# Kernel optimization log

Measured on AMD Instinct MI355X. Metric: run time of the kernel, lower is better.

Reference implementation:

```python
import jax, jax.numpy as jnp
import numpy as np

N_NODES, N_EDGES, D_IN, N_GRAPHS = 20000, 320000, 256, 32
H1, C1, H2, C2 = 4, 128, 4, 64


def setup_inputs() -> dict:
    key = jax.random.key(0)
    ks = jax.random.split(key, 24)
    g = lambda k, shape, fan: jax.random.normal(k, shape, jnp.float32) * (1.0 / np.sqrt(fan))
    inp = {
        'x': jax.random.normal(ks[0], (N_NODES, D_IN), jnp.float32),
        'edge_index': jax.random.randint(ks[1], (2, N_EDGES), 0, N_NODES, jnp.int32),
        'batch': jnp.sort(jax.random.randint(ks[2], (N_NODES,), 0, N_GRAPHS, jnp.int32)),
        'edge_attr': jax.random.normal(ks[3], (N_EDGES, 1), jnp.float32),
        # GATConv 1: lin [D_IN, H1*C1], att_src/dst/edge [H1,C1], lin_edge [1,H1*C1], bias [H1*C1]
        'W1': g(ks[4], (D_IN, H1 * C1), D_IN),
        'as1': g(ks[5], (H1, C1), C1),
        'ad1': g(ks[6], (H1, C1), C1),
        'We1': g(ks[7], (1, H1 * C1), 1),
        'ae1': g(ks[8], (H1, C1), C1),
        'b1': jnp.zeros((H1 * C1,), jnp.float32),
        'g1': jnp.ones((H1 * C1,), jnp.float32),
        'be1': jnp.zeros((H1 * C1,), jnp.float32),
        # GATConv 2 (concat=False -> out 64)
        'W2': g(ks[9], (H1 * C1, H2 * C2), H1 * C1),
        'as2': g(ks[10], (H2, C2), C2),
        'ad2': g(ks[11], (H2, C2), C2),
        'We2': g(ks[12], (1, H2 * C2), 1),
        'ae2': g(ks[13], (H2, C2), C2),
        'b2': jnp.zeros((C2,), jnp.float32),
        'g2': jnp.ones((C2,), jnp.float32),
        'be2': jnp.zeros((C2,), jnp.float32),
        'fw1': g(ks[14], (C2, 32), C2),
        'fb1': jnp.zeros((32,), jnp.float32),
        'fw2': g(ks[15], (32, 1), 32),
        'fb2': jnp.zeros((1,), jnp.float32),
    }
    return inp


def _gat(x, src, dst, ea, W, a_s, a_d, We, a_e, bias, H, C, concat, n):
    h = (x @ W).reshape(n, H, C)                         # [N,H,C]
    al_s = jnp.einsum('nhc,hc->nh', h, a_s)              # [N,H]
    al_d = jnp.einsum('nhc,hc->nh', h, a_d)
    e = (ea @ We).reshape(-1, H, C)                      # [E',H,C]
    al_e = jnp.einsum('ehc,hc->eh', e, a_e)
    logits = jax.nn.leaky_relu(al_s[src] + al_d[dst] + al_e, 0.2)  # [E',H]
    m = jax.ops.segment_max(logits, dst, num_segments=n)
    m = jnp.where(jnp.isfinite(m), m, 0.0)
    p = jnp.exp(logits - m[dst])
    denom = jax.ops.segment_sum(p, dst, num_segments=n)
    alpha = p / (denom[dst] + 1e-16)                     # segment softmax
    out = jax.ops.segment_sum(h[src] * alpha[:, :, None], dst, num_segments=n)
    out = out.reshape(n, H * C) if concat else out.mean(axis=1)
    return out + bias


def _bn(x, gamma, beta):
    mu = x.mean(axis=0)
    var = x.var(axis=0)
    return gamma * (x - mu) * jax.lax.rsqrt(var + 1e-5) + beta


def reference(x, edge_index, batch, edge_attr, W1, as1, ad1, We1, ae1, b1, g1, be1,
              W2, as2, ad2, We2, ae2, b2, g2, be2, fw1, fb1, fw2, fb2):
    n = x.shape[0]
    loop = jnp.arange(n, dtype=edge_index.dtype)
    src = jnp.concatenate([edge_index[0], loop])
    dst = jnp.concatenate([edge_index[1], loop])
    # self-loop edge_attr filled with mean (PyG fill_value='mean')
    ea = jnp.concatenate([edge_attr, jnp.broadcast_to(edge_attr.mean(axis=0), (n, edge_attr.shape[1]))])

    h = _gat(x, src, dst, ea, W1, as1, ad1, We1, ae1, b1, H1, C1, True, n)
    h = jax.nn.elu(_bn(h, g1, be1))
    h = _gat(h, src, dst, ea, W2, as2, ad2, We2, ae2, b2, H2, C2, False, n)
    h = jax.nn.elu(_bn(h, g2, be2))

    sums = jax.ops.segment_sum(h, batch, num_segments=N_GRAPHS)
    cnt = jax.ops.segment_sum(jnp.ones((n,), h.dtype), batch, num_segments=N_GRAPHS)
    pooled = sums / jnp.maximum(cnt, 1.0)[:, None]       # global_mean_pool
    # dropout is identity in eval mode
    out = jax.nn.elu(pooled @ fw1 + fb1) @ fw2 + fb2
    return out
```

## Files before the change

kernel.cpp:

```cpp
#include <hip/hip_runtime.h>
#include <hip/hip_bf16.h>

#define N_NODES  20000
#define MPAD     20096
#define N_EDGES  320000
#define N_EP     (N_EDGES + N_NODES)
#define D_IN     256
#define N_GRAPHS 32
#define HH1 4
#define CC1 128
#define HH2 4
#define CC2 64

#define R1_OFF     0ull
#define R2_OFF     41156608ull
#define XB_OFF     61734912ull
#define ALPHA_OFF  72024064ull
#define EAF_OFF    77464064ull
#define W1BT_OFF   78744064ull
#define W2BT_OFF   79006208ull
#define CSR_OFF    79268352ull
#define DEG_OFF    81988352ull
#define MUSUM_OFF  82068352ull
#define M2SUM_OFF  82070400ull
#define POOL_OFF   82072448ull
#define FLAGZ_OFF  82080640ull
#define EAACC_OFF  82080768ull
#define ZERO0_START DEG_OFF
#define ZERO0_SIZE  92480ull
#define ROWPTR_OFF 82080832ull
#define ALS_OFF    82160896ull
#define ALD_OFF    82480896ull
#define MU_OFF     82800896ull
#define RSTD_OFF   82802944ull
#define SBUF_OFF   82804992ull
#define SMALL_OFF  82805056ull
#define H1_OFF     R1_OFF
#define OUT1_OFF   R1_OFF
#define H2_OFF     R1_OFF
#define HB2_OFF    (R1_OFF + 20578304ull)
#define HB1_OFF    R2_OFF
#define OUT1B_OFF  R2_OFF
#define OUT2A_OFF  R2_OFF
#define OUT2_OFF   ALPHA_OFF

#define S_AS1 0
#define S_AD1 512
#define S_WE1 1024
#define S_AE1 1536
#define S_G1  2048
#define S_BE1 2560
#define S_AS2 3072
#define S_AD2 3328
#define S_WE2 3584
#define S_AE2 3840
#define S_G2  4096
#define S_BE2 4160
#define S_FW1 4224
#define S_FB1 6272
#define S_FW2 6304
#define S_FB2 6336

typedef __attribute__((ext_vector_type(8))) short bf8_t;
typedef __attribute__((ext_vector_type(4))) float f4_t;

__global__ void detect_dtype(const unsigned short* __restrict__ xr, int* __restrict__ flag) {
    int i = blockIdx.x * blockDim.x + threadIdx.x;
    unsigned short u = xr[i];
    if ((u & 0x7F80) == 0x7F80) atomicOr(flag, 1);
}

__device__ __forceinline__ float loadF(const void* p, int i, int fp32) {
    return fp32 ? ((const float*)p)[i]
                : __bfloat162float(((const __hip_bfloat16*)p)[i]);
}

__global__ void cvt_big(const int* __restrict__ flag, const void* __restrict__ src,
                        float* __restrict__ dst, int n) {
    int fp32 = flag[0];
    for (int i = blockIdx.x * blockDim.x + threadIdx.x; i < n; i += gridDim.x * blockDim.x)
        dst[i] = loadF(src, i, fp32);
}

__global__ void cvt_to_bf16(const int* __restrict__ flag, const void* __restrict__ src,
                            __hip_bfloat16* __restrict__ dst, int n_valid, int n_total) {
    int i = blockIdx.x * blockDim.x + threadIdx.x;
    if (i >= n_total) return;
    float v = (i < n_valid) ? loadF(src, i, flag[0]) : 0.f;
    dst[i] = __float2bfloat16(v);
}

__global__ void cvt_w_t(const int* __restrict__ flag, const void* __restrict__ W,
                        __hip_bfloat16* __restrict__ Wt, int K, int N) {
    int i = blockIdx.x * blockDim.x + threadIdx.x;
    if (i >= K * N) return;
    int k = i / N, n = i % N;
    Wt[(size_t)n * K + k] = __float2bfloat16(loadF(W, i, flag[0]));
}

__global__ void cvt_smalls(const int* __restrict__ flag, float* __restrict__ dst,
                           const void* as1, const void* ad1, const void* We1, const void* ae1,
                           const void* g1, const void* be1, const void* as2, const void* ad2,
                           const void* We2, const void* ae2, const void* g2, const void* be2,
                           const void* fw1, const void* fb1, const void* fw2, const void* fb2) {
    const void* srcs[16] = {as1, ad1, We1, ae1, g1, be1, as2, ad2, We2, ae2, g2, be2, fw1, fb1, fw2, fb2};
    const int cnts[16] = {512, 512, 512, 512, 512, 512, 256, 256, 256, 256, 64, 64, 2048, 32, 32, 1};
    const int offs[16] = {S_AS1, S_AD1, S_WE1, S_AE1, S_G1, S_BE1, S_AS2, S_AD2,
                          S_WE2, S_AE2, S_G2, S_BE2, S_FW1, S_FB1, S_FW2, S_FB2};
    int b = blockIdx.x;
    int fp32 = flag[0];
    for (int i = threadIdx.x; i < cnts[b]; i += blockDim.x)
        dst[offs[b] + i] = loadF(srcs[b], i, fp32);
}

__global__ void ea_reduce(const float* __restrict__ ea, float* __restrict__ acc) {
    __shared__ float sh[256];
    float s = 0.f;
    for (int i = blockIdx.x * blockDim.x + threadIdx.x; i < N_EDGES; i += gridDim.x * blockDim.x)
        s += ea[i];
    sh[threadIdx.x] = s;
    __syncthreads();
    for (int st = 128; st; st >>= 1) {
        if (threadIdx.x < st) sh[threadIdx.x] += sh[threadIdx.x + st];
        __syncthreads();
    }
    if (threadIdx.x == 0) atomicAdd(acc, sh[0]);
}

__global__ void compute_s(const float* __restrict__ smalls, float* __restrict__ sbuf) {
    int t = threadIdx.x;
    if (t < 4) {
        float s = 0.f;
        for (int c = 0; c < CC1; ++c) s += smalls[S_WE1 + t * CC1 + c] * smalls[S_AE1 + t * CC1 + c];
        sbuf[t] = s;
    } else if (t < 8) {
        int h = t - 4;
        float s = 0.f;
        for (int c = 0; c < CC2; ++c) s += smalls[S_WE2 + h * CC2 + c] * smalls[S_AE2 + h * CC2 + c];
        sbuf[t] = s;
    }
}

__global__ void edge_hist(const int* __restrict__ ei, int* __restrict__ deg) {
    int e = blockIdx.x * blockDim.x + threadIdx.x;
    if (e >= N_EP) return;
    int d = (e < N_EDGES) ? ei[N_EDGES + e] : e - N_EDGES;
    atomicAdd(&deg[d], 1);
}

__global__ void deg_scan(const int* __restrict__ deg, int* __restrict__ rowptr) {
    __shared__ int part[256];
    int t = threadIdx.x;
    int lo = t * 79;
    int hi = lo + 79; if (hi > N_NODES) hi = N_NODES; if (lo > N_NODES) lo = N_NODES;
    int s = 0;
    for (int i = lo; i < hi; ++i) s += deg[i];
    part[t] = s;
    __syncthreads();
    for (int off = 1; off < 256; off <<= 1) {
        int u = (t >= off) ? part[t - off] : 0;
        __syncthreads();
        if (t >= off) part[t] += u;
        __syncthreads();
    }
    int run = part[t] - s;
    for (int i = lo; i < hi; ++i) { rowptr[i] = run; run += deg[i]; }
    if (hi == N_NODES && lo < N_NODES) rowptr[N_NODES] = run;
}

__global__ void edge_scatter(const int* __restrict__ ei, const int* __restrict__ rowptr,
                             int* __restrict__ cursor, int2* __restrict__ csr_se) {
    int e = blockIdx.x * blockDim.x + threadIdx.x;
    if (e >= N_EP) return;
    int s, d;
    if (e < N_EDGES) { s = ei[e]; d = ei[N_EDGES + e]; }
    else { s = d = e - N_EDGES; }
    int pos = rowptr[d] + atomicAdd(&cursor[d], 1);
    csr_se[pos] = make_int2(s, e);
}

__global__ void graph_bounds(const int* __restrict__ batch, int* __restrict__ gstart) {
    int i = blockIdx.x * blockDim.x + threadIdx.x;
    if (i >= N_NODES) return;
    int b = batch[i];
    if (i == 0) {
        for (int g = 0; g <= b; ++g) gstart[g] = 0;
    } else {
        int pb = batch[i - 1];
        for (int g = pb + 1; g <= b; ++g) gstart[g] = i;
    }
    if (i == N_NODES - 1) {
        for (int g = b + 1; g <= N_GRAPHS; ++g) gstart[g] = N_NODES;
    }
}

__global__ __launch_bounds__(256) void gemm_mfma(
        const short* __restrict__ A, const short* __restrict__ Bt,
        float* __restrict__ C, __hip_bfloat16* __restrict__ Cb, int N, int K) {
    __shared__ short As[128 * 40];
    __shared__ short Bs[64 * 40];
    int t = threadIdx.x;
    int wv = t >> 6, lane = t & 63, quad = lane >> 4, lr = lane & 15;
    int m0 = blockIdx.y * 128, n0 = blockIdx.x * 64;
    f4_t acc[2][4] = {};
    int ra0 = t >> 2, sa0 = t & 3;
    int ra1 = (t + 256) >> 2, sa1 = t & 3;
    for (int k0 = 0; k0 < K; k0 += 32) {
        *(uint4*)&As[ra0 * 40 + sa0 * 8] = *(const uint4*)&A[(size_t)(m0 + ra0) * K + k0 + sa0 * 8];
        *(uint4*)&As[ra1 * 40 + sa1 * 8] = *(const uint4*)&A[(size_t)(m0 + ra1) * K + k0 + sa1 * 8];
        *(uint4*)&Bs[ra0 * 40 + sa0 * 8] = *(const uint4*)&Bt[(size_t)(n0 + ra0) * K + k0 + sa0 * 8];
        __syncthreads();
        bf8_t a0 = *(const bf8_t*)&As[(wv * 16 + lr) * 40 + quad * 8];
        bf8_t a1 = *(const bf8_t*)&As[((wv + 4) * 16 + lr) * 40 + quad * 8];
#pragma unroll
        for (int nt = 0; nt < 4; ++nt) {
            bf8_t b = *(const bf8_t*)&Bs[(nt * 16 + lr) * 40 + quad * 8];
            acc[0][nt] = __builtin_amdgcn_mfma_f32_16x16x32_bf16(a0, b, acc[0][nt], 0, 0, 0);
            acc[1][nt] = __builtin_amdgcn_mfma_f32_16x16x32_bf16(a1, b, acc[1][nt], 0, 0, 0);
        }
        __syncthreads();
    }
#pragma unroll
    for (int si = 0; si < 2; ++si) {
        int mrow = m0 + (wv + si * 4) * 16 + quad * 4;
#pragma unroll
        for (int nt = 0; nt < 4; ++nt) {
            int col = n0 + nt * 16 + lr;
#pragma unroll
            for (int r = 0; r < 4; ++r) {
                float v = acc[si][nt][r];
                C[(size_t)(mrow + r) * N + col] = v;
                Cb[(size_t)(mrow + r) * N + col] = __float2bfloat16(v);
            }
        }
    }
}

__global__ void al_kernel(const float* __restrict__ hbuf, const float* __restrict__ smalls,
                          int s_as, int s_ad,
                          float* __restrict__ als, float* __restrict__ ald, int H, int C) {
    int n = blockIdx.x;
    int lane = threadIdx.x;
    int HC = H * C;
    for (int h = 0; h < H; ++h) {
        float ss = 0.f, sd = 0.f;
        for (int c = lane; c < C; c += 64) {
            float v = hbuf[(size_t)n * HC + h * C + c];
            ss += v * smalls[s_as + h * C + c];
            sd += v * smalls[s_ad + h * C + c];
        }
        for (int off = 32; off; off >>= 1) {
            ss += __shfl_down(ss, off);
            sd += __shfl_down(sd, off);
        }
        if (lane == 0) { als[n * H + h] = ss; ald[n * H + h] = sd; }
    }
}

__global__ __launch_bounds__(64) void edge_softmax_csr(
        const int* __restrict__ rowptr, const int2* __restrict__ csr_se,
        const float* __restrict__ als, const float* __restrict__ ald,
        const float* __restrict__ eaf, const float* __restrict__ ea_acc,
        const float* __restrict__ sbuf, float* __restrict__ alpha) {
    int d = blockIdx.x;
    int lane = threadIdx.x;
    int beg = rowptr[d], end = rowptr[d + 1];
    float ea_mean = ea_acc[0] * (1.0f / N_EDGES);
    float4 ad = *(const float4*)&ald[d * 4];
    float s0 = sbuf[0], s1 = sbuf[1], s2 = sbuf[2], s3 = sbuf[3];
    float m0 = -INFINITY, m1 = -INFINITY, m2 = -INFINITY, m3 = -INFINITY;
    for (int p = beg + lane; p < end; p += 64) {
        int2 se = csr_se[p];
        float eav = (se.y < N_EDGES) ? eaf[se.y] : ea_mean;
        float4 as = *(const float4*)&als[se.x * 4];
        float l0 = as.x + ad.x + eav * s0; l0 = l0 > 0.f ? l0 : 0.2f * l0;
        float l1 = as.y + ad.y + eav * s1; l1 = l1 > 0.f ? l1 : 0.2f * l1;
        float l2 = as.z + ad.z + eav * s2; l2 = l2 > 0.f ? l2 : 0.2f * l2;
        float l3 = as.w + ad.w + eav * s3; l3 = l3 > 0.f ? l3 : 0.2f * l3;
        float4 lv = {l0, l1, l2, l3};
        *(float4*)&alpha[(size_t)p * 4] = lv;
        m0 = fmaxf(m0, l0); m1 = fmaxf(m1, l1); m2 = fmaxf(m2, l2); m3 = fmaxf(m3, l3);
    }
#pragma unroll
    for (int off = 1; off < 64; off <<= 1) {
        m0 = fmaxf(m0, __shfl_xor(m0, off));
        m1 = fmaxf(m1, __shfl_xor(m1, off));
        m2 = fmaxf(m2, __shfl_xor(m2, off));
        m3 = fmaxf(m3, __shfl_xor(m3, off));
    }
    float t0 = 0.f, t1 = 0.f, t2 = 0.f, t3 = 0.f;
    for (int p = beg + lane; p < end; p += 64) {
        float4 lv = *(const float4*)&alpha[(size_t)p * 4];
        lv.x = __expf(lv.x - m0); lv.y = __expf(lv.y - m1);
        lv.z = __expf(lv.z - m2); lv.w = __expf(lv.w - m3);
        *(float4*)&alpha[(size_t)p * 4] = lv;
        t0 += lv.x; t1 += lv.y; t2 += lv.z; t3 += lv.w;
    }
#pragma unroll
    for (int off = 1; off < 64; off <<= 1) {
        t0 += __shfl_xor(t0, off);
        t1 += __shfl_xor(t1, off);
        t2 += __shfl_xor(t2, off);
        t3 += __shfl_xor(t3, off);
    }
    float r0 = 1.0f / (t0 + 1e-16f), r1 = 1.0f / (t1 + 1e-16f);
    float r2 = 1.0f / (t2 + 1e-16f), r3 = 1.0f / (t3 + 1e-16f);
    for (int p = beg + lane; p < end; p += 64) {
        float4 lv = *(const float4*)&alpha[(size_t)p * 4];
        lv.x *= r0; lv.y *= r1; lv.z *= r2; lv.w *= r3;
        *(float4*)&alpha[(size_t)p * 4] = lv;
    }
}

template <int HC, int C>
__global__ __launch_bounds__(HC / 4) void agg_csr_bf(
        const int* __restrict__ rowptr, const int2* __restrict__ csr_se,
        const float* __restrict__ alpha, const __hip_bfloat16* __restrict__ hb,
        float* __restrict__ outb) {
    int d = blockIdx.x;
    int t = threadIdx.x;
    int h = (4 * t) / C;
    float a0 = 0.f, a1 = 0.f, a2 = 0.f, a3 = 0.f;
    int beg = rowptr[d], end = rowptr[d + 1];
    for (int p = beg; p < end; ++p) {
        int2 se = csr_se[p];
        float w = alpha[(size_t)p * 4 + h];
        uint2 raw = *(const uint2*)&hb[(size_t)se.x * HC + 4 * t];
        a0 += w * __uint_as_float(raw.x << 16);
        a1 += w * __uint_as_float(raw.x & 0xFFFF0000u);
        a2 += w * __uint_as_float(raw.y << 16);
        a3 += w * __uint_as_float(raw.y & 0xFFFF0000u);
    }
    float4 v = {a0, a1, a2, a3};
    *(float4*)&outb[(size_t)d * HC + 4 * t] = v;
}

__global__ void bn_part(const float* __restrict__ x, float* __restrict__ musum, float* __restrict__ m2sum, int Cc) {
    int c = threadIdx.x;
    float s = 0.f, s2 = 0.f;
    for (int i = blockIdx.x; i < N_NODES; i += gridDim.x) {
        float v = x[(size_t)i * Cc + c];
        s += v; s2 += v * v;
    }
    atomicAdd(&musum[c], s);
    atomicAdd(&m2sum[c], s2);
}

__global__ void bn_fin(float* __restrict__ musum, float* __restrict__ m2sum,
                       float* __restrict__ mu, float* __restrict__ rstd, int Cc) {
    int c = threadIdx.x;
    if (c >= Cc) return;
    float m = musum[c] / N_NODES;
    float var = m2sum[c] / N_NODES - m * m;
    mu[c] = m;
    rstd[c] = rsqrtf(var + 1e-5f);
    musum[c] = 0.f;
    m2sum[c] = 0.f;
}

__global__ void bn_apply_elu_b(const float* __restrict__ x, const float* __restrict__ mu,
                               const float* __restrict__ rstd, const float* __restrict__ smalls,
                               int s_g, int s_be, __hip_bfloat16* __restrict__ out,
                               int total, int Cc) {
    int i = blockIdx.x * blockDim.x + threadIdx.x;
    if (i >= total) return;
    int j = i % Cc;
    float y = smalls[s_g + j] * (x[i] - mu[j]) * rstd[j] + smalls[s_be + j];
    y = y > 0.f ? y : expm1f(y);
    out[i] = __float2bfloat16(y);
}

__global__ void bn_apply_elu(float* __restrict__ x, const float* __restrict__ mu, const float* __restrict__ rstd,
                             const float* __restrict__ smalls, int s_g, int s_be,
                             int total, int Cc) {
    int i = blockIdx.x * blockDim.x + threadIdx.x;
    if (i >= total) return;
    int j = i % Cc;
    float y = smalls[s_g + j] * (x[i] - mu[j]) * rstd[j] + smalls[s_be + j];
    x[i] = y > 0.f ? y : expm1f(y);
}

__global__ void head_mean(const float* __restrict__ ina, float* __restrict__ outb) {
    int i = blockIdx.x * blockDim.x + threadIdx.x;
    if (i >= N_NODES * CC2) return;
    int nd = i / CC2, c = i % CC2;
    float s = 0.f;
#pragma unroll
    for (int h = 0; h < HH2; ++h) s += ina[(size_t)nd * (HH2 * CC2) + h * CC2 + c];
    outb[i] = s * (1.0f / HH2);
}

__global__ __launch_bounds__(256) void pool_seg(const float* __restrict__ x, const int* __restrict__ gstart,
                                                float* __restrict__ pooled) {
    int g = blockIdx.x;
    int c = threadIdx.x & 63;
    int j = threadIdx.x >> 6;
    int beg = gstart[g], end = gstart[g + 1];
    float s = 0.f;
    for (int i = beg + j; i < end; i += 4)
        s += x[(size_t)i * CC2 + c];
    __shared__ float sh[4][64];
    sh[j][c] = s;
    __syncthreads();
    if (j == 0) {
        float tot = sh[0][c] + sh[1][c] + sh[2][c] + sh[3][c];
        float n = (float)(end - beg);
        pooled[g * CC2 + c] = tot / fmaxf(n, 1.0f);
    }
}

__global__ void mlp_kernel(const float* __restrict__ pooled,
                           const float* __restrict__ smalls, const int* __restrict__ flag,
                           void* __restrict__ outp) {
    int g = blockIdx.x;
    int k = threadIdx.x;
    __shared__ float hsh[32];
    float acc = smalls[S_FB1 + k];
    for (int c = 0; c < CC2; ++c)
        acc += pooled[g * CC2 + c] * smalls[S_FW1 + c * 32 + k];
    acc = acc > 0.f ? acc : expm1f(acc);
    hsh[k] = acc;
    __syncthreads();
    if (k == 0) {
        float o = smalls[S_FB2];
        for (int t = 0; t < 32; ++t) o += hsh[t] * smalls[S_FW2 + t];
        if (flag[0]) ((float*)outp)[g] = o;
        else ((__hip_bfloat16*)outp)[g] = __float2bfloat16(o);
    }
}

extern "C" void kernel_launch(void* const* d_in, const int* in_sizes, int n_in,
                              void* d_out, int out_size, void* d_ws, size_t ws_size,
                              hipStream_t stream) {
    const void* x    = d_in[0];
    const int* ei    = (const int*)d_in[1];
    const int* batch = (const int*)d_in[2];
    const void* ea   = d_in[3];
    const void* W1   = d_in[4];
    const void* as1  = d_in[5];
    const void* ad1  = d_in[6];
    const void* We1  = d_in[7];
    const void* ae1  = d_in[8];
    const void* g1   = d_in[10];
    const void* be1  = d_in[11];
    const void* W2   = d_in[12];
    const void* as2  = d_in[13];
    const void* ad2  = d_in[14];
    const void* We2  = d_in[15];
    const void* ae2  = d_in[16];
    const void* g2   = d_in[18];
    const void* be2  = d_in[19];
    const void* fw1  = d_in[20];
    const void* fb1  = d_in[21];
    const void* fw2  = d_in[22];
    const void* fb2  = d_in[23];

    char* ws = (char*)d_ws;
    float* h1      = (float*)(ws + H1_OFF);
    float* out1    = (float*)(ws + OUT1_OFF);
    float* h2      = (float*)(ws + H2_OFF);
    __hip_bfloat16* hb1   = (__hip_bfloat16*)(ws + HB1_OFF);
    __hip_bfloat16* hb2   = (__hip_bfloat16*)(ws + HB2_OFF);
    __hip_bfloat16* out1b = (__hip_bfloat16*)(ws + OUT1B_OFF);
    __hip_bfloat16* xb    = (__hip_bfloat16*)(ws + XB_OFF);
    __hip_bfloat16* W1bt  = (__hip_bfloat16*)(ws + W1BT_OFF);
    __hip_bfloat16* W2bt  = (__hip_bfloat16*)(ws + W2BT_OFF);
    float* out2a   = (float*)(ws + OUT2A_OFF);
    float* out2    = (float*)(ws + OUT2_OFF);
    float* alpha   = (float*)(ws + ALPHA_OFF);
    float* eaf     = (float*)(ws + EAF_OFF);
    int2*  csr_se  = (int2*)(ws + CSR_OFF);
    int*   deg     = (int*)(ws + DEG_OFF);
    float* musum   = (float*)(ws + MUSUM_OFF);
    float* m2sum   = (float*)(ws + M2SUM_OFF);
    float* pooled  = (float*)(ws + POOL_OFF);
    int*   flag    = (int*)(ws + FLAGZ_OFF);
    float* ea_acc  = (float*)(ws + EAACC_OFF);
    int*   rowptr  = (int*)(ws + ROWPTR_OFF);
    float* als     = (float*)(ws + ALS_OFF);
    float* ald     = (float*)(ws + ALD_OFF);
    float* mu      = (float*)(ws + MU_OFF);
    float* rstd    = (float*)(ws + RSTD_OFF);
    float* sbuf    = (float*)(ws + SBUF_OFF);
    float* smalls  = (float*)(ws + SMALL_OFF);
    int*   gstart  = (int*)(ws + DEG_OFF);

    hipMemsetAsync(ws + ZERO0_START, 0, ZERO0_SIZE, stream);

    detect_dtype<<<256, 256, 0, stream>>>((const unsigned short*)x, flag);
    cvt_to_bf16<<<(MPAD * D_IN + 255) / 256, 256, 0, stream>>>(flag, x, xb, N_NODES * D_IN, MPAD * D_IN);
    cvt_big<<<1250, 256, 0, stream>>>(flag, ea, eaf, N_EDGES);
    cvt_w_t<<<512, 256, 0, stream>>>(flag, W1, W1bt, D_IN, HH1 * CC1);
    cvt_w_t<<<512, 256, 0, stream>>>(flag, W2, W2bt, HH1 * CC1, HH2 * CC2);
    cvt_smalls<<<16, 256, 0, stream>>>(flag, smalls, as1, ad1, We1, ae1, g1, be1,
                                       as2, ad2, We2, ae2, g2, be2, fw1, fb1, fw2, fb2);

    ea_reduce<<<256, 256, 0, stream>>>(eaf, ea_acc);
    compute_s<<<1, 64, 0, stream>>>(smalls, sbuf);

    int eb = (N_EP + 255) / 256;
    edge_hist<<<eb, 256, 0, stream>>>(ei, deg);
    deg_scan<<<1, 256, 0, stream>>>(deg, rowptr);
    hipMemsetAsync(ws + DEG_OFF, 0, 80000, stream);
    edge_scatter<<<eb, 256, 0, stream>>>(ei, rowptr, deg, csr_se);
    graph_bounds<<<(N_NODES + 255) / 256, 256, 0, stream>>>(batch, gstart);

    gemm_mfma<<<dim3(512 / 64, MPAD / 128), 256, 0, stream>>>(
        (const short*)xb, (const short*)W1bt, h1, hb1, 512, 256);
    al_kernel<<<N_NODES, 64, 0, stream>>>(h1, smalls, S_AS1, S_AD1, als, ald, HH1, CC1);
    edge_softmax_csr<<<N_NODES, 64, 0, stream>>>(rowptr, csr_se, als, ald, eaf, ea_acc, sbuf, alpha);
    agg_csr_bf<512, 128><<<N_NODES, 128, 0, stream>>>(rowptr, csr_se, alpha, hb1, out1);

    bn_part<<<256, 512, 0, stream>>>(out1, musum, m2sum, 512);
    bn_fin<<<1, 512, 0, stream>>>(musum, m2sum, mu, rstd, 512);
    bn_apply_elu_b<<<(N_NODES * 512 + 255) / 256, 256, 0, stream>>>(
        out1, mu, rstd, smalls, S_G1, S_BE1, out1b, N_NODES * 512, 512);

    gemm_mfma<<<dim3(256 / 64, MPAD / 128), 256, 0, stream>>>(
        (const short*)out1b, (const short*)W2bt, h2, hb2, 256, 512);
    al_kernel<<<N_NODES, 64, 0, stream>>>(h2, smalls, S_AS2, S_AD2, als, ald, HH2, CC2);
    edge_softmax_csr<<<N_NODES, 64, 0, stream>>>(rowptr, csr_se, als, ald, eaf, ea_acc, sbuf + 4, alpha);
    agg_csr_bf<256, 64><<<N_NODES, 64, 0, stream>>>(rowptr, csr_se, alpha, hb2, out2a);

    head_mean<<<(N_NODES * CC2 + 255) / 256, 256, 0, stream>>>(out2a, out2);
    bn_part<<<256, 64, 0, stream>>>(out2, musum, m2sum, 64);
    bn_fin<<<1, 64, 0, stream>>>(musum, m2sum, mu, rstd, 64);
    bn_apply_elu<<<(N_NODES * 64 + 255) / 256, 256, 0, stream>>>(out2, mu, rstd, smalls, S_G2, S_BE2, N_NODES * 64, 64);

    pool_seg<<<N_GRAPHS, 256, 0, stream>>>(out2, gstart, pooled);
    mlp_kernel<<<N_GRAPHS, 32, 0, stream>>>(pooled, smalls, flag, d_out);
}
```

Before: 516.1 us.

## Fuse prep, attention-logit, normalization and pooling kernels; drop fp32 intermediates

Merges the many conversion kernels into one prep launch, folds the attention-logit dot products into the GEMM epilogue through atomics, and moves softmax normalization into the aggregation step, which removes the alpha rewrite pass. Layer-1 aggregation and batchnorm now run on bf16 buffers instead of fp32. The BN finalize step is folded into apply, and pooling is fused with the MLP. The aim is fewer launches and less memory traffic, at the cost of atomic contention in the GEMM epilogue and reduced precision in the intermediates.

```diff
diff --git a/kernel.cpp b/kernel.cpp
--- a/kernel.cpp
+++ b/kernel.cpp
@@ -12,37 +12,36 @@
 #define HH2 4
 #define CC2 64
 
-#define R1_OFF     0ull
-#define R2_OFF     41156608ull
-#define XB_OFF     61734912ull
-#define ALPHA_OFF  72024064ull
-#define EAF_OFF    77464064ull
-#define W1BT_OFF   78744064ull
-#define W2BT_OFF   79006208ull
-#define CSR_OFF    79268352ull
-#define DEG_OFF    81988352ull
-#define MUSUM_OFF  82068352ull
-#define M2SUM_OFF  82070400ull
-#define POOL_OFF   82072448ull
-#define FLAGZ_OFF  82080640ull
-#define EAACC_OFF  82080768ull
+#define XB_OFF      0ull
+#define HB1_OFF     10289152ull
+#define AGG1_OFF    30867456ull
+#define HB2_OFF     51445760ull
+#define OUT2A_OFF   61734912ull
+#define OUT2_OFF    82214912ull
+#define ALPHA_OFF   87334912ull
+#define DENOM_OFF   92774912ull
+#define EAF_OFF     93094912ull
+#define W1BT_OFF    94374912ull
+#define W2BT_OFF    94637056ull
+#define CSR_OFF     94899200ull
+#define ROWPTR_OFF  97619200ull
+#define GSTART_OFF  97699264ull
+#define SMALL_OFF   97699520ull
+#define SBUF_OFF    97725120ull
+#define DEG_OFF     97725184ull
+#define CURS_OFF    97805184ull
+#define ALS1_OFF    97885184ull
+#define ALD1_OFF    98206720ull
+#define ALS2_OFF    98528256ull
+#define ALD2_OFF    98849792ull
+#define MUSUM1_OFF  99171328ull
+#define M2SUM1_OFF  99173376ull
+#define MUSUM2_OFF  99175424ull
+#define M2SUM2_OFF  99175936ull
+#define FLAGZ_OFF   99176448ull
+#define EAACC_OFF   99176576ull
 #define ZERO0_START DEG_OFF
-#define ZERO0_SIZE  92480ull
-#define ROWPTR_OFF 82080832ull
-#define ALS_OFF    82160896ull
-#define ALD_OFF    82480896ull
-#define MU_OFF     82800896ull
-#define RSTD_OFF   82802944ull
-#define SBUF_OFF   82804992ull
-#define SMALL_OFF  82805056ull
-#define H1_OFF     R1_OFF
-#define OUT1_OFF   R1_OFF
-#define H2_OFF     R1_OFF
-#define HB2_OFF    (R1_OFF + 20578304ull)
-#define HB1_OFF    R2_OFF
-#define OUT1B_OFF  R2_OFF
-#define OUT2A_OFF  R2_OFF
-#define OUT2_OFF   ALPHA_OFF
+#define ZERO0_SIZE  1451456ull
 
 #define S_AS1 0
 #define S_AD1 512
@@ -75,89 +74,125 @@
                 : __bfloat162float(((const __hip_bfloat16*)p)[i]);
 }
 
-__global__ void cvt_big(const int* __restrict__ flag, const void* __restrict__ src,
-                        float* __restrict__ dst, int n) {
+#define PB_XB  5024
+#define PB_EAF 313
+#define PB_W   512
+#define PB_SM  16
+#define PREP_BLOCKS (PB_XB + PB_EAF + 2 * PB_W + PB_SM + 1)
+__global__ __launch_bounds__(256) void prep(
+        const int* __restrict__ flag,
+        const void* x, const void* ea, const void* W1, const void* W2,
+        const void* as1, const void* ad1, const void* We1, const void* ae1,
+        const void* g1, const void* be1, const void* as2, const void* ad2,
+        const void* We2, const void* ae2, const void* g2, const void* be2,
+        const void* fw1, const void* fb1, const void* fw2, const void* fb2,
+        __hip_bfloat16* __restrict__ xb, float* __restrict__ eaf, float* __restrict__ ea_acc,
+        __hip_bfloat16* __restrict__ W1bt, __hip_bfloat16* __restrict__ W2bt,
+        float* __restrict__ smalls, float* __restrict__ sbuf) {
+    __shared__ float sh[256];
+    int b = blockIdx.x, t = threadIdx.x;
     int fp32 = flag[0];
-    for (int i = blockIdx.x * blockDim.x + threadIdx.x; i < n; i += gridDim.x * blockDim.x)
-        dst[i] = loadF(src, i, fp32);
-}
-
-__global__ void cvt_to_bf16(const int* __restrict__ flag, const void* __restrict__ src,
-                            __hip_bfloat16* __restrict__ dst, int n_valid, int n_total) {
-    int i = blockIdx.x * blockDim.x + threadIdx.x;
-    if (i >= n_total) return;
-    float v = (i < n_valid) ? loadF(src, i, flag[0]) : 0.f;
-    dst[i] = __float2bfloat16(v);
-}
-
-__global__ void cvt_w_t(const int* __restrict__ flag, const void* __restrict__ W,
-                        __hip_bfloat16* __restrict__ Wt, int K, int N) {
-    int i = blockIdx.x * blockDim.x + threadIdx.x;
-    if (i >= K * N) return;
-    int k = i / N, n = i % N;
-    Wt[(size_t)n * K + k] = __float2bfloat16(loadF(W, i, flag[0]));
-}
-
-__global__ void cvt_smalls(const int* __restrict__ flag, float* __restrict__ dst,
-                           const void* as1, const void* ad1, const void* We1, const void* ae1,
-                           const void* g1, const void* be1, const void* as2, const void* ad2,
-                           const void* We2, const void* ae2, const void* g2, const void* be2,
-                           const void* fw1, const void* fb1, const void* fw2, const void* fb2) {
-    const void* srcs[16] = {as1, ad1, We1, ae1, g1, be1, as2, ad2, We2, ae2, g2, be2, fw1, fb1, fw2, fb2};
-    const int cnts[16] = {512, 512, 512, 512, 512, 512, 256, 256, 256, 256, 64, 64, 2048, 32, 32, 1};
-    const int offs[16] = {S_AS1, S_AD1, S_WE1, S_AE1, S_G1, S_BE1, S_AS2, S_AD2,
-                          S_WE2, S_AE2, S_G2, S_BE2, S_FW1, S_FB1, S_FW2, S_FB2};
-    int b = blockIdx.x;
-    int fp32 = flag[0];
-    for (int i = threadIdx.x; i < cnts[b]; i += blockDim.x)
-        dst[offs[b] + i] = loadF(srcs[b], i, fp32);
-}
-
-__global__ void ea_reduce(const float* __restrict__ ea, float* __restrict__ acc) {
-    __shared__ float sh[256];
-    float s = 0.f;
-    for (int i = blockIdx.x * blockDim.x + threadIdx.x; i < N_EDGES; i += gridDim.x * blockDim.x)
-        s += ea[i];
-    sh[threadIdx.x] = s;
-    __syncthreads();
-    for (int st = 128; st; st >>= 1) {
-        if (threadIdx.x < st) sh[threadIdx.x] += sh[threadIdx.x + st];
+    if (b < PB_XB) {
+        int base = (b * 256 + t) * 4;
+        __hip_bfloat16 tmp[4];
+#pragma unroll
+        for (int j = 0; j < 4; ++j) {
+            int i = base + j;
+            float v = (i < N_NODES * D_IN) ? loadF(x, i, fp32) : 0.f;
+            tmp[j] = __float2bfloat16(v);
+        }
+        *(uint2*)&xb[base] = *(uint2*)tmp;
+        return;
+    }
+    b -= PB_XB;
+    if (b < PB_EAF) {
+        int base = (b * 256 + t) * 4;
+        float s = 0.f;
+#pragma unroll
+        for (int j = 0; j < 4; ++j) {
+            int i = base + j;
+            if (i < N_EDGES) { float v = loadF(ea, i, fp32); eaf[i] = v; s += v; }
+        }
+        sh[t] = s;
         __syncthreads();
-    }
-    if (threadIdx.x == 0) atomicAdd(acc, sh[0]);
-}
-
-__global__ void compute_s(const float* __restrict__ smalls, float* __restrict__ sbuf) {
-    int t = threadIdx.x;
+        for (int st = 128; st; st >>= 1) {
+            if (t < st) sh[t] += sh[t + st];
+            __syncthreads();
+        }
+        if (t == 0) atomicAdd(ea_acc, sh[0]);
+        return;
+    }
+    b -= PB_EAF;
+    if (b < PB_W) {
+        int i = b * 256 + t;
+        int k = i >> 9, n = i & 511;
+        W1bt[(size_t)n * 256 + k] = __float2bfloat16(loadF(W1, i, fp32));
+        return;
+    }
+    b -= PB_W;
+    if (b < PB_W) {
+        int i = b * 256 + t;
+        int k = i >> 8, n = i & 255;
+        W2bt[(size_t)n * 512 + k] = __float2bfloat16(loadF(W2, i, fp32));
+        return;
+    }
+    b -= PB_W;
+    if (b < PB_SM) {
+        const void* srcs[16] = {as1, ad1, We1, ae1, g1, be1, as2, ad2, We2, ae2, g2, be2, fw1, fb1, fw2, fb2};
+        const int cnts[16] = {512, 512, 512, 512, 512, 512, 256, 256, 256, 256, 64, 64, 2048, 32, 32, 1};
+        const int offs[16] = {S_AS1, S_AD1, S_WE1, S_AE1, S_G1, S_BE1, S_AS2, S_AD2,
+                              S_WE2, S_AE2, S_G2, S_BE2, S_FW1, S_FB1, S_FW2, S_FB2};
+        for (int i = t; i < cnts[b]; i += 256)
+            smalls[offs[b] + i] = loadF(srcs[b], i, fp32);
+        return;
+    }
     if (t < 4) {
         float s = 0.f;
-        for (int c = 0; c < CC1; ++c) s += smalls[S_WE1 + t * CC1 + c] * smalls[S_AE1 + t * CC1 + c];
+        for (int c = 0; c < CC1; ++c) s += loadF(We1, t * CC1 + c, fp32) * loadF(ae1, t * CC1 + c, fp32);
         sbuf[t] = s;
     } else if (t < 8) {
         int h = t - 4;
         float s = 0.f;
-        for (int c = 0; c < CC2; ++c) s += smalls[S_WE2 + h * CC2 + c] * smalls[S_AE2 + h * CC2 + c];
-        sbuf[t] = s;
-    }
-}
-
-__global__ void edge_hist(const int* __restrict__ ei, int* __restrict__ deg) {
-    int e = blockIdx.x * blockDim.x + threadIdx.x;
-    if (e >= N_EP) return;
-    int d = (e < N_EDGES) ? ei[N_EDGES + e] : e - N_EDGES;
-    atomicAdd(&deg[d], 1);
-}
-
-__global__ void deg_scan(const int* __restrict__ deg, int* __restrict__ rowptr) {
-    __shared__ int part[256];
+        for (int c = 0; c < CC2; ++c) s += loadF(We2, h * CC2 + c, fp32) * loadF(ae2, h * CC2 + c, fp32);
+        sbuf[4 + h] = s;
+    }
+}
+
+#define HIST_BLOCKS 1329
+__global__ void hist_bounds(const int* __restrict__ ei, int* __restrict__ deg,
+                            const int* __restrict__ batch, int* __restrict__ gstart) {
+    int b = blockIdx.x, t = threadIdx.x;
+    if (b < HIST_BLOCKS) {
+        int e = b * 256 + t;
+        if (e >= N_EP) return;
+        int d = (e < N_EDGES) ? ei[N_EDGES + e] : e - N_EDGES;
+        atomicAdd(&deg[d], 1);
+        return;
+    }
+    int i = (b - HIST_BLOCKS) * 256 + t;
+    if (i >= N_NODES) return;
+    int bb = batch[i];
+    if (i == 0) {
+        for (int g = 0; g <= bb; ++g) gstart[g] = 0;
+    } else {
+        int pb = batch[i - 1];
+        for (int g = pb + 1; g <= bb; ++g) gstart[g] = i;
+    }
+    if (i == N_NODES - 1) {
+        for (int g = bb + 1; g <= N_GRAPHS; ++g) gstart[g] = N_NODES;
+    }
+}
+
+__global__ __launch_bounds__(1024) void deg_scan(const int* __restrict__ deg, int* __restrict__ rowptr) {
+    __shared__ int part[1024];
     int t = threadIdx.x;
-    int lo = t * 79;
-    int hi = lo + 79; if (hi > N_NODES) hi = N_NODES; if (lo > N_NODES) lo = N_NODES;
+    int lo = t * 20;
+    int hi = lo + 20; if (hi > N_NODES) hi = N_NODES; if (lo > N_NODES) lo = N_NODES;
     int s = 0;
     for (int i = lo; i < hi; ++i) s += deg[i];
     part[t] = s;
     __syncthreads();
-    for (int off = 1; off < 256; off <<= 1) {
+    for (int off = 1; off < 1024; off <<= 1) {
         int u = (t >= off) ? part[t - off] : 0;
         __syncthreads();
         if (t >= off) part[t] += u;
@@ -179,24 +214,11 @@
     csr_se[pos] = make_int2(s, e);
 }
 
-__global__ void graph_bounds(const int* __restrict__ batch, int* __restrict__ gstart) {
-    int i = blockIdx.x * blockDim.x + threadIdx.x;
-    if (i >= N_NODES) return;
-    int b = batch[i];
-    if (i == 0) {
-        for (int g = 0; g <= b; ++g) gstart[g] = 0;
-    } else {
-        int pb = batch[i - 1];
-        for (int g = pb + 1; g <= b; ++g) gstart[g] = i;
-    }
-    if (i == N_NODES - 1) {
-        for (int g = b + 1; g <= N_GRAPHS; ++g) gstart[g] = N_NODES;
-    }
-}
-
-__global__ __launch_bounds__(256) void gemm_mfma(
+__global__ __launch_bounds__(256) void gemm_mfma_al(
         const short* __restrict__ A, const short* __restrict__ Bt,
-        float* __restrict__ C, __hip_bfloat16* __restrict__ Cb, int N, int K) {
+        __hip_bfloat16* __restrict__ Cb, int N, int K,
+        float* __restrict__ als, float* __restrict__ ald,
+        const float* __restrict__ asv, const float* __restrict__ adv, int cshift) {
     __shared__ short As[128 * 40];
     __shared__ short Bs[64 * 40];
     int t = threadIdx.x;
@@ -204,10 +226,10 @@
     int m0 = blockIdx.y * 128, n0 = blockIdx.x * 64;
     f4_t acc[2][4] = {};
     int ra0 = t >> 2, sa0 = t & 3;
-    int ra1 = (t + 256) >> 2, sa1 = t & 3;
+    int ra1 = (t + 256) >> 2;
     for (int k0 = 0; k0 < K; k0 += 32) {
         *(uint4*)&As[ra0 * 40 + sa0 * 8] = *(const uint4*)&A[(size_t)(m0 + ra0) * K + k0 + sa0 * 8];
-        *(uint4*)&As[ra1 * 40 + sa1 * 8] = *(const uint4*)&A[(size_t)(m0 + ra1) * K + k0 + sa1 * 8];
+        *(uint4*)&As[ra1 * 40 + sa0 * 8] = *(const uint4*)&A[(size_t)(m0 + ra1) * K + k0 + sa0 * 8];
         *(uint4*)&Bs[ra0 * 40 + sa0 * 8] = *(const uint4*)&Bt[(size_t)(n0 + ra0) * K + k0 + sa0 * 8];
         __syncthreads();
         bf8_t a0 = *(const bf8_t*)&As[(wv * 16 + lr) * 40 + quad * 8];
@@ -227,33 +249,38 @@
         for (int nt = 0; nt < 4; ++nt) {
             int col = n0 + nt * 16 + lr;
 #pragma unroll
-            for (int r = 0; r < 4; ++r) {
-                float v = acc[si][nt][r];
-                C[(size_t)(mrow + r) * N + col] = v;
-                Cb[(size_t)(mrow + r) * N + col] = __float2bfloat16(v);
+            for (int r = 0; r < 4; ++r)
+                Cb[(size_t)(mrow + r) * N + col] = __float2bfloat16(acc[si][nt][r]);
+        }
+    }
+    float asv4[4], adv4[4];
+#pragma unroll
+    for (int nt = 0; nt < 4; ++nt) {
+        asv4[nt] = asv[n0 + nt * 16 + lr];
+        adv4[nt] = adv[n0 + nt * 16 + lr];
+    }
+    int hsel = n0 >> cshift;
+#pragma unroll
+    for (int si = 0; si < 2; ++si) {
+#pragma unroll
+        for (int r = 0; r < 4; ++r) {
+            float ps = 0.f, pd = 0.f;
+#pragma unroll
+            for (int nt = 0; nt < 4; ++nt) {
+                ps += acc[si][nt][r] * asv4[nt];
+                pd += acc[si][nt][r] * adv4[nt];
+            }
+#pragma unroll
+            for (int m = 1; m < 16; m <<= 1) {
+                ps += __shfl_xor(ps, m);
+                pd += __shfl_xor(pd, m);
+            }
+            if (lr == 0) {
+                int row = m0 + (wv + si * 4) * 16 + quad * 4 + r;
+                atomicAdd(&als[row * 4 + hsel], ps);
+                atomicAdd(&ald[row * 4 + hsel], pd);
             }
         }
-    }
-}
-
-__global__ void al_kernel(const float* __restrict__ hbuf, const float* __restrict__ smalls,
-                          int s_as, int s_ad,
-                          float* __restrict__ als, float* __restrict__ ald, int H, int C) {
-    int n = blockIdx.x;
-    int lane = threadIdx.x;
-    int HC = H * C;
-    for (int h = 0; h < H; ++h) {
-        float ss = 0.f, sd = 0.f;
-        for (int c = lane; c < C; c += 64) {
-            float v = hbuf[(size_t)n * HC + h * C + c];
-            ss += v * smalls[s_as + h * C + c];
-            sd += v * smalls[s_ad + h * C + c];
-        }
-        for (int off = 32; off; off >>= 1) {
-            ss += __shfl_down(ss, off);
-            sd += __shfl_down(sd, off);
-        }
-        if (lane == 0) { als[n * H + h] = ss; ald[n * H + h] = sd; }
     }
 }
 
@@ -261,7 +288,7 @@
         const int* __restrict__ rowptr, const int2* __restrict__ csr_se,
         const float* __restrict__ als, const float* __restrict__ ald,
         const float* __restrict__ eaf, const float* __restrict__ ea_acc,
-        const float* __restrict__ sbuf, float* __restrict__ alpha) {
+        const float* __restrict__ sbuf, float* __restrict__ alpha, float* __restrict__ denom) {
     int d = blockIdx.x;
     int lane = threadIdx.x;
     int beg = rowptr[d], end = rowptr[d + 1];
@@ -303,23 +330,21 @@
         t2 += __shfl_xor(t2, off);
         t3 += __shfl_xor(t3, off);
     }
-    float r0 = 1.0f / (t0 + 1e-16f), r1 = 1.0f / (t1 + 1e-16f);
-    float r2 = 1.0f / (t2 + 1e-16f), r3 = 1.0f / (t3 + 1e-16f);
-    for (int p = beg + lane; p < end; p += 64) {
-        float4 lv = *(const float4*)&alpha[(size_t)p * 4];
-        lv.x *= r0; lv.y *= r1; lv.z *= r2; lv.w *= r3;
-        *(float4*)&alpha[(size_t)p * 4] = lv;
-    }
-}
-
-template <int HC, int C>
+    if (lane == 0) {
+        float4 dn = {t0, t1, t2, t3};
+        *(float4*)&denom[d * 4] = dn;
+    }
+}
+
+template <int HC, int C, bool B16OUT>
 __global__ __launch_bounds__(HC / 4) void agg_csr_bf(
         const int* __restrict__ rowptr, const int2* __restrict__ csr_se,
-        const float* __restrict__ alpha, const __hip_bfloat16* __restrict__ hb,
-        float* __restrict__ outb) {
+        const float* __restrict__ alpha, const float* __restrict__ denom,
+        const __hip_bfloat16* __restrict__ hb, void* __restrict__ outb) {
     int d = blockIdx.x;
     int t = threadIdx.x;
     int h = (4 * t) / C;
+    float rdn = 1.0f / (denom[d * (HC / C) + h] + 1e-16f);
     float a0 = 0.f, a1 = 0.f, a2 = 0.f, a3 = 0.f;
     int beg = rowptr[d], end = rowptr[d + 1];
     for (int p = beg; p < end; ++p) {
@@ -331,99 +356,118 @@
         a2 += w * __uint_as_float(raw.y << 16);
         a3 += w * __uint_as_float(raw.y & 0xFFFF0000u);
     }
-    float4 v = {a0, a1, a2, a3};
-    *(float4*)&outb[(size_t)d * HC + 4 * t] = v;
-}
-
-__global__ void bn_part(const float* __restrict__ x, float* __restrict__ musum, float* __restrict__ m2sum, int Cc) {
-    int c = threadIdx.x;
-    float s = 0.f, s2 = 0.f;
+    a0 *= rdn; a1 *= rdn; a2 *= rdn; a3 *= rdn;
+    if (B16OUT) {
+        __hip_bfloat16 tmp[4] = {__float2bfloat16(a0), __float2bfloat16(a1),
+                                 __float2bfloat16(a2), __float2bfloat16(a3)};
+        *(uint2*)&((__hip_bfloat16*)outb)[(size_t)d * HC + 4 * t] = *(uint2*)tmp;
+    } else {
+        float4 v = {a0, a1, a2, a3};
+        *(float4*)&((float*)outb)[(size_t)d * HC + 4 * t] = v;
+    }
+}
+
+__global__ __launch_bounds__(256) void bn_part_b(const __hip_bfloat16* __restrict__ x,
+                                                 float* __restrict__ musum, float* __restrict__ m2sum) {
+    int t = threadIdx.x;
+    float s0 = 0.f, s20 = 0.f, s1 = 0.f, s21 = 0.f;
     for (int i = blockIdx.x; i < N_NODES; i += gridDim.x) {
-        float v = x[(size_t)i * Cc + c];
-        s += v; s2 += v * v;
-    }
-    atomicAdd(&musum[c], s);
-    atomicAdd(&m2sum[c], s2);
-}
-
-__global__ void bn_fin(float* __restrict__ musum, float* __restrict__ m2sum,
-                       float* __restrict__ mu, float* __restrict__ rstd, int Cc) {
-    int c = threadIdx.x;
-    if (c >= Cc) return;
-    float m = musum[c] / N_NODES;
-    float var = m2sum[c] / N_NODES - m * m;
-    mu[c] = m;
-    rstd[c] = rsqrtf(var + 1e-5f);
-    musum[c] = 0.f;
-    m2sum[c] = 0.f;
-}
-
-__global__ void bn_apply_elu_b(const float* __restrict__ x, const float* __restrict__ mu,
-                               const float* __restrict__ rstd, const float* __restrict__ smalls,
-                               int s_g, int s_be, __hip_bfloat16* __restrict__ out,
-                               int total, int Cc) {
+        unsigned u = *(const unsigned*)&x[(size_t)i * 512 + 2 * t];
+        float v0 = __uint_as_float(u << 16);
+        float v1 = __uint_as_float(u & 0xFFFF0000u);
+        s0 += v0; s20 += v0 * v0; s1 += v1; s21 += v1 * v1;
+    }
+    atomicAdd(&musum[2 * t], s0);
+    atomicAdd(&m2sum[2 * t], s20);
+    atomicAdd(&musum[2 * t + 1], s1);
+    atomicAdd(&m2sum[2 * t + 1], s21);
+}
+
+__global__ __launch_bounds__(256) void bn_apply_elu_b16(__hip_bfloat16* __restrict__ x,
+                                                        const float* __restrict__ musum,
+                                                        const float* __restrict__ m2sum,
+                                                        const float* __restrict__ smalls) {
+    int q = blockIdx.x * blockDim.x + threadIdx.x;
+    if (q >= N_NODES * 512 / 4) return;
+    int base = q * 4;
+    int j = base & 511;
+    uint2 raw = *(uint2*)&x[base];
+    float v[4] = {__uint_as_float(raw.x << 16), __uint_as_float(raw.x & 0xFFFF0000u),
+                  __uint_as_float(raw.y << 16), __uint_as_float(raw.y & 0xFFFF0000u)};
+    __hip_bfloat16 tmp[4];
+#pragma unroll
+    for (int k = 0; k < 4; ++k) {
+        int jj = j + k;
+        float m = musum[jj] * (1.0f / N_NODES);
+        float var = m2sum[jj] * (1.0f / N_NODES) - m * m;
+        float y = smalls[S_G1 + jj] * (v[k] - m) * rsqrtf(var + 1e-5f) + smalls[S_BE1 + jj];
+        y = y > 0.f ? y : expm1f(y);
+        tmp[k] = __float2bfloat16(y);
+    }
+    *(uint2*)&x[base] = *(uint2*)tmp;
+}
+
+__global__ __launch_bounds__(256) void head_mean_stats(const float* __restrict__ ina, float* __restrict__ outb,
+                                                       float* __restrict__ musum, float* __restrict__ m2sum) {
+    int t = threadIdx.x;
+    int c = t & 63, j = t >> 6;
+    float ls = 0.f, ls2 = 0.f;
+    for (int nd = blockIdx.x * 4 + j; nd < N_NODES; nd += gridDim.x * 4) {
+        size_t base = (size_t)nd * 256 + c;
+        float s = (ina[base] + ina[base + 64] + ina[base + 128] + ina[base + 192]) * 0.25f;
+        outb[(size_t)nd * 64 + c] = s;
+        ls += s; ls2 += s * s;
+    }
+    __shared__ float shs[4][64], sh2[4][64];
+    shs[j][c] = ls; sh2[j][c] = ls2;
+    __syncthreads();
+    if (j == 0) {
+        atomicAdd(&musum[c], shs[0][c] + shs[1][c] + shs[2][c] + shs[3][c]);
+        atomicAdd(&m2sum[c], sh2[0][c] + sh2[1][c] + sh2[2][c] + sh2[3][c]);
+    }
+}
+
+__global__ void bn_apply_elu_f32(float* __restrict__ x, const float* __restrict__ musum,
+                                 const float* __restrict__ m2sum, const float* __restrict__ smalls) {
     int i = blockIdx.x * blockDim.x + threadIdx.x;
-    if (i >= total) return;
-    int j = i % Cc;
-    float y = smalls[s_g + j] * (x[i] - mu[j]) * rstd[j] + smalls[s_be + j];
-    y = y > 0.f ? y : expm1f(y);
-    out[i] = __float2bfloat16(y);
-}
-
-__global__ void bn_apply_elu(float* __restrict__ x, const float* __restrict__ mu, const float* __restrict__ rstd,
-                             const float* __restrict__ smalls, int s_g, int s_be,
-                             int total, int Cc) {
-    int i = blockIdx.x * blockDim.x + threadIdx.x;
-    if (i >= total) return;
-    int j = i % Cc;
-    float y = smalls[s_g + j] * (x[i] - mu[j]) * rstd[j] + smalls[s_be + j];
+    if (i >= N_NODES * 64) return;
+    int j = i & 63;
+    float m = musum[j] * (1.0f / N_NODES);
+    float var = m2sum[j] * (1.0f / N_NODES) - m * m;
+    float y = smalls[S_G2 + j] * (x[i] - m) * rsqrtf(var + 1e-5f) + smalls[S_BE2 + j];
     x[i] = y > 0.f ? y : expm1f(y);
 }
 
-__global__ void head_mean(const float* __restrict__ ina, float* __restrict__ outb) {
-    int i = blockIdx.x * blockDim.x + threadIdx.x;
-    if (i >= N_NODES * CC2) return;
-    int nd = i / CC2, c = i % CC2;
-    float s = 0.f;
-#pragma unroll
-    for (int h = 0; h < HH2; ++h) s += ina[(size_t)nd * (HH2 * CC2) + h * CC2 + c];
-    outb[i] = s * (1.0f / HH2);
-}
-
-__global__ __launch_bounds__(256) void pool_seg(const float* __restrict__ x, const int* __restrict__ gstart,
-                                                float* __restrict__ pooled) {
+__global__ __launch_bounds__(256) void pool_mlp(const float* __restrict__ x, const int* __restrict__ gstart,
+                                                const float* __restrict__ smalls, const int* __restrict__ flag,
+                                                void* __restrict__ outp) {
     int g = blockIdx.x;
-    int c = threadIdx.x & 63;
-    int j = threadIdx.x >> 6;
+    int t = threadIdx.x;
+    int c = t & 63, j = t >> 6;
     int beg = gstart[g], end = gstart[g + 1];
     float s = 0.f;
     for (int i = beg + j; i < end; i += 4)
-        s += x[(size_t)i * CC2 + c];
+        s += x[(size_t)i * 64 + c];
     __shared__ float sh[4][64];
+    __shared__ float pooled[64];
+    __shared__ float hsh[32];
     sh[j][c] = s;
     __syncthreads();
     if (j == 0) {
         float tot = sh[0][c] + sh[1][c] + sh[2][c] + sh[3][c];
-        float n = (float)(end - beg);
-        pooled[g * CC2 + c] = tot / fmaxf(n, 1.0f);
-    }
-}
-
-__global__ void mlp_kernel(const float* __restrict__ pooled,
-                           const float* __restrict__ smalls, const int* __restrict__ flag,
-                           void* __restrict__ outp) {
-    int g = blockIdx.x;
-    int k = threadIdx.x;
-    __shared__ float hsh[32];
-    float acc = smalls[S_FB1 + k];
-    for (int c = 0; c < CC2; ++c)
-        acc += pooled[g * CC2 + c] * smalls[S_FW1 + c * 32 + k];
-    acc = acc > 0.f ? acc : expm1f(acc);
-    hsh[k] = acc;
+        pooled[c] = tot / fmaxf((float)(end - beg), 1.0f);
+    }
     __syncthreads();
-    if (k == 0) {
+    if (t < 32) {
+        float acc = smalls[S_FB1 + t];
+        for (int cc = 0; cc < 64; ++cc)
+            acc += pooled[cc] * smalls[S_FW1 + cc * 32 + t];
+        hsh[t] = acc > 0.f ? acc : expm1f(acc);
+    }
+    __syncthreads();
+    if (t == 0) {
         float o = smalls[S_FB2];
-        for (int t = 0; t < 32; ++t) o += hsh[t] * smalls[S_FW2 + t];
+        for (int k = 0; k < 32; ++k) o += hsh[k] * smalls[S_FW2 + k];
         if (flag[0]) ((float*)outp)[g] = o;
         else ((__hip_bfloat16*)outp)[g] = __float2bfloat16(o);
     }
@@ -456,77 +500,63 @@
     const void* fb2  = d_in[23];
 
     char* ws = (char*)d_ws;
-    float* h1      = (float*)(ws + H1_OFF);
-    float* out1    = (float*)(ws + OUT1_OFF);
-    float* h2      = (float*)(ws + H2_OFF);
-    __hip_bfloat16* hb1   = (__hip_bfloat16*)(ws + HB1_OFF);
-    __hip_bfloat16* hb2   = (__hip_bfloat16*)(ws + HB2_OFF);
-    __hip_bfloat16* out1b = (__hip_bfloat16*)(ws + OUT1B_OFF);
-    __hip_bfloat16* xb    = (__hip_bfloat16*)(ws + XB_OFF);
-    __hip_bfloat16* W1bt  = (__hip_bfloat16*)(ws + W1BT_OFF);
-    __hip_bfloat16* W2bt  = (__hip_bfloat16*)(ws + W2BT_OFF);
-    float* out2a   = (float*)(ws + OUT2A_OFF);
-    float* out2    = (float*)(ws + OUT2_OFF);
-    float* alpha   = (float*)(ws + ALPHA_OFF);
-    float* eaf     = (float*)(ws + EAF_OFF);
-    int2*  csr_se  = (int2*)(ws + CSR_OFF);
-    int*   deg     = (int*)(ws + DEG_OFF);
-    float* musum   = (float*)(ws + MUSUM_OFF);
-    float* m2sum   = (float*)(ws + M2SUM_OFF);
-    float* pooled  = (float*)(ws + POOL_OFF);
-    int*   flag    = (int*)(ws + FLAGZ_OFF);
-    float* ea_acc  = (float*)(ws + EAACC_OFF);
-    int*   rowptr  = (int*)(ws + ROWPTR_OFF);
-    float* als     = (float*)(ws + ALS_OFF);
-    float* ald     = (float*)(ws + ALD_OFF);
-    float* mu      = (float*)(ws + MU_OFF);
-    float* rstd    = (float*)(ws + RSTD_OFF);
-    float* sbuf    = (float*)(ws + SBUF_OFF);
-    float* smalls  = (float*)(ws + SMALL_OFF);
-    int*   gstart  = (int*)(ws + DEG_OFF);
+    __hip_bfloat16* xb   = (__hip_bfloat16*)(ws + XB_OFF);
+    __hip_bfloat16* hb1  = (__hip_bfloat16*)(ws + HB1_OFF);
+    __hip_bfloat16* agg1 = (__hip_bfloat16*)(ws + AGG1_OFF);
+    __hip_bfloat16* hb2  = (__hip_bfloat16*)(ws + HB2_OFF);
+    float* out2a  = (float*)(ws + OUT2A_OFF);
+    float* out2   = (float*)(ws + OUT2_OFF);
+    float* alpha  = (float*)(ws + ALPHA_OFF);
+    float* denom  = (float*)(ws + DENOM_OFF);
+    float* eaf    = (float*)(ws + EAF_OFF);
+    __hip_bfloat16* W1bt = (__hip_bfloat16*)(ws + W1BT_OFF);
+    __hip_bfloat16* W2bt = (__hip_bfloat16*)(ws + W2BT_OFF);
+    int2*  csr_se = (int2*)(ws + CSR_OFF);
+    int*   rowptr = (int*)(ws + ROWPTR_OFF);
+    int*   gstart = (int*)(ws + GSTART_OFF);
+    float* smalls = (float*)(ws + SMALL_OFF);
+    float* sbuf   = (float*)(ws + SBUF_OFF);
+    int*   deg    = (int*)(ws + DEG_OFF);
+    int*   cursor = (int*)(ws + CURS_OFF);
+    float* als1   = (float*)(ws + ALS1_OFF);
+    float* ald1   = (float*)(ws + ALD1_OFF);
+    float* als2   = (float*)(ws + ALS2_OFF);
+    float* ald2   = (float*)(ws + ALD2_OFF);
+    float* musum1 = (float*)(ws + MUSUM1_OFF);
+    float* m2sum1 = (float*)(ws + M2SUM1_OFF);
+    float* musum2 = (float*)(ws + MUSUM2_OFF);
+    float* m2sum2 = (float*)(ws + M2SUM2_OFF);
+    int*   flag   = (int*)(ws + FLAGZ_OFF);
+    float* ea_acc = (float*)(ws + EAACC_OFF);
 
     hipMemsetAsync(ws + ZERO0_START, 0, ZERO0_SIZE, stream);
+    hipMemsetAsync(ws + AGG1_OFF + (size_t)N_NODES * 512 * 2, 0, (MPAD - N_NODES) * 512 * 2, stream);
 
     detect_dtype<<<256, 256, 0, stream>>>((const unsigned short*)x, flag);
-    cvt_to_bf16<<<(MPAD * D_IN + 255) / 256, 256, 0, stream>>>(flag, x, xb, N_NODES * D_IN, MPAD * D_IN);
-    cvt_big<<<1250, 256, 0, stream>>>(flag, ea, eaf, N_EDGES);
-    cvt_w_t<<<512, 256, 0, stream>>>(flag, W1, W1bt, D_IN, HH1 * CC1);
-    cvt_w_t<<<512, 256, 0, stream>>>(flag, W2, W2bt, HH1 * CC1, HH2 * CC2);
-    cvt_smalls<<<16, 256, 0, stream>>>(flag, smalls, as1, ad1, We1, ae1, g1, be1,
-                                       as2, ad2, We2, ae2, g2, be2, fw1, fb1, fw2, fb2);
-
-    ea_reduce<<<256, 256, 0, stream>>>(eaf, ea_acc);
-    compute_s<<<1, 64, 0, stream>>>(smalls, sbuf);
-
-    int eb = (N_EP + 255) / 256;
-    edge_hist<<<eb, 256, 0, stream>>>(ei, deg);
-    deg_scan<<<1, 256, 0, stream>>>(deg, rowptr);
-    hipMemsetAsync(ws + DEG_OFF, 0, 80000, stream);
-    edge_scatter<<<eb, 256, 0, stream>>>(ei, rowptr, deg, csr_se);
-    graph_bounds<<<(N_NODES + 255) / 256, 256, 0, stream>>>(batch, gstart);
-
-    gemm_mfma<<<dim3(512 / 64, MPAD / 128), 256, 0, stream>>>(
-        (const short*)xb, (const short*)W1bt, h1, hb1, 512, 256);
-    al_kernel<<<N_NODES, 64, 0, stream>>>(h1, smalls, S_AS1, S_AD1, als, ald, HH1, CC1);
-    edge_softmax_csr<<<N_NODES, 64, 0, stream>>>(rowptr, csr_se, als, ald, eaf, ea_acc, sbuf, alpha);
-    agg_csr_bf<512, 128><<<N_NODES, 128, 0, stream>>>(rowptr, csr_se, alpha, hb1, out1);
-
-    bn_part<<<256, 512, 0, stream>>>(out1, musum, m2sum, 512);
-    bn_fin<<<1, 512, 0, stream>>>(musum, m2sum, mu, rstd, 512);
-    bn_apply_elu_b<<<(N_NODES * 512 + 255) / 256, 256, 0, stream>>>(
-        out1, mu, rstd, smalls, S_G1, S_BE1, out1b, N_NODES * 512, 512);
-
-    gemm_mfma<<<dim3(256 / 64, MPAD / 128), 256, 0, stream>>>(
-        (const short*)out1b, (const short*)W2bt, h2, hb2, 256, 512);
-    al_kernel<<<N_NODES, 64, 0, stream>>>(h2, smalls, S_AS2, S_AD2, als, ald, HH2, CC2);
-    edge_softmax_csr<<<N_NODES, 64, 0, stream>>>(rowptr, csr_se, als, ald, eaf, ea_acc, sbuf + 4, alpha);
-    agg_csr_bf<256, 64><<<N_NODES, 64, 0, stream>>>(rowptr, csr_se, alpha, hb2, out2a);
-
-    head_mean<<<(N_NODES * CC2 + 255) / 256, 256, 0, stream>>>(out2a, out2);
-    bn_part<<<256, 64, 0, stream>>>(out2, musum, m2sum, 64);
-    bn_fin<<<1, 64, 0, stream>>>(musum, m2sum, mu, rstd, 64);
-    bn_apply_elu<<<(N_NODES * 64 + 255) / 256, 256, 0, stream>>>(out2, mu, rstd, smalls, S_G2, S_BE2, N_NODES * 64, 64);
-
-    pool_seg<<<N_GRAPHS, 256, 0, stream>>>(out2, gstart, pooled);
-    mlp_kernel<<<N_GRAPHS, 32, 0, stream>>>(pooled, smalls, flag, d_out);
-}
+    prep<<<PREP_BLOCKS, 256, 0, stream>>>(flag, x, ea, W1, W2,
+                                          as1, ad1, We1, ae1, g1, be1, as2, ad2,
+                                          We2, ae2, g2, be2, fw1, fb1, fw2, fb2,
+                                          xb, eaf, ea_acc, W1bt, W2bt, smalls, sbuf);
+
+    hist_bounds<<<HIST_BLOCKS + 79, 256, 0, stream>>>(ei, deg, batch, gstart);
+    deg_scan<<<1, 1024, 0, stream>>>(deg, rowptr);
+    edge_scatter<<<HIST_BLOCKS, 256, 0, stream>>>(ei, rowptr, cursor, csr_se);
+
+    gemm_mfma_al<<<dim3(512 / 64, MPAD / 128), 256, 0, stream>>>(
+        (const short*)xb, (const short*)W1bt, hb1, 512, 256,
+        als1, ald1, smalls + S_AS1, smalls + S_AD1, 7);
+    edge_softmax_csr<<<N_NODES, 64, 0, stream>>>(rowptr, csr_se, als1, ald1, eaf, ea_acc, sbuf, alpha, denom);
+    agg_csr_bf<512, 128, true><<<N_NODES, 128, 0, stream>>>(rowptr, csr_se, alpha, denom, hb1, agg1);
+    bn_part_b<<<256, 256, 0, stream>>>(agg1, musum1, m2sum1);
+    bn_apply_elu_b16<<<10000, 256, 0, stream>>>(agg1, musum1, m2sum1, smalls);
+
+    gemm_mfma_al<<<dim3(256 / 64, MPAD / 128), 256, 0, stream>>>(
+        (const short*)agg1, (const short*)W2bt, hb2, 256, 512,
+        als2, ald2, smalls + S_AS2, smalls + S_AD2, 6);
+    edge_softmax_csr<<<N_NODES, 64, 0, stream>>>(rowptr, csr_se, als2, ald2, eaf, ea_acc, sbuf + 4, alpha, denom);
+    agg_csr_bf<256, 64, false><<<N_NODES, 64, 0, stream>>>(rowptr, csr_se, alpha, denom, hb2, out2a);
+    head_mean_stats<<<256, 256, 0, stream>>>(out2a, out2, musum2, m2sum2);
+    bn_apply_elu_f32<<<(N_NODES * 64 + 255) / 256, 256, 0, stream>>>(out2, musum2, m2sum2, smalls);
+
+    pool_mlp<<<N_GRAPHS, 256, 0, stream>>>(out2, gstart, smalls, flag, d_out);
+}
```

Result: faster. 496.3 us (-3.8%).
